# Kernel optimization log

Hardware: AMD Instinct MI355X
Metric: run time of the kernel (lower is better)

The kernel has to match this reference:

```python
import jax, jax.numpy as jnp
import numpy as np

M, H = 7, 200                 # ensemble size, hidden width
OBS, ACT = 32, 8
C = OBS + ACT                 # model input dim
DOUT = OBS + 1                # next-obs delta + reward
N = 100000                    # number of transitions
E_NUM = 5                     # number of elites
MAX_LOGVAR, MIN_LOGVAR = 0.5, -10.0
REWARD_SCALE, REWARD_BIAS = 1.0, 0.0
TERM_THRESH = 50.0


def setup_inputs() -> dict:
    key = jax.random.key(0)
    ks = jax.random.split(key, 10)
    def w(k, shape, fan_in):
        return jax.random.normal(k, shape, jnp.float32) / np.float32(np.sqrt(fan_in))
    return {
        "observations": jax.random.normal(ks[0], (N, OBS), jnp.float32),
        "actions": jax.random.normal(ks[1], (N, ACT), jnp.float32),
        "scaler_mu": jax.random.normal(ks[2], (C,), jnp.float32) * 0.1,
        "scaler_std": jax.random.uniform(ks[3], (C,), jnp.float32, 0.5, 1.5),
        "W1": w(ks[4], (M, C, H), C), "b1": jnp.zeros((M, 1, H), jnp.float32),
        "W2": w(ks[5], (M, H, H), H), "b2": jnp.zeros((M, 1, H), jnp.float32),
        "W3": w(ks[6], (M, H, H), H), "b3": jnp.zeros((M, 1, H), jnp.float32),
        "W4": w(ks[7], (M, H, 2 * DOUT), H), "b4": jnp.zeros((M, 1, 2 * DOUT), jnp.float32),
        "elites": jnp.arange(E_NUM, dtype=jnp.int32),
    }


def _ensemble_mlp(z, W1, b1, W2, b2, W3, b3, W4, b4):
    # z: [M, R, C] -> mean, logvar: [M, R, DOUT]
    h = jax.nn.swish(jnp.einsum('mrc,mch->mrh', z, W1) + b1)
    h = jax.nn.swish(jnp.einsum('mrh,mhk->mrk', h, W2) + b2)
    h = jax.nn.swish(jnp.einsum('mrh,mhk->mrk', h, W3) + b3)
    out = jnp.einsum('mrh,mhk->mrk', h, W4) + b4
    mean, logvar = out[..., :DOUT], out[..., DOUT:]
    logvar = MAX_LOGVAR - jax.nn.softplus(MAX_LOGVAR - logvar)
    logvar = MIN_LOGVAR + jax.nn.softplus(logvar - MIN_LOGVAR)
    return mean, logvar


def _terminal_fn(observations, actions, next_obs):
    # simple environment-style terminal predicate, shape [N, 1]
    return jnp.linalg.norm(next_obs, axis=-1, keepdims=True) > TERM_THRESH


def reference(observations, actions, scaler_mu, scaler_std,
              W1, b1, W2, b2, W3, b3, W4, b4, elites):
    key = jax.random.key(0)  # source uses the SAME key for permutation and noise
    z = jnp.concatenate([observations, actions], axis=1)
    z = (z - scaler_mu) / scaler_std
    n, c = z.shape
    e = elites.shape[0]
    r = (n - 1) // e + 1
    pad = e * r - n
    z = jnp.concatenate([z, jnp.zeros((pad, c), z.dtype)], axis=0)
    idxs = jax.random.permutation(key, e * r)
    tmp = z[idxs].reshape(e, r, c)                    # dispatch to elite slots
    zf = jnp.zeros((M, r, c), z.dtype).at[elites].set(tmp)
    mean, logvar = _ensemble_mlp(zf, W1, b1, W2, b2, W3, b3, W4, b4)
    std = jnp.exp(0.5 * logvar)
    ensemble_samples = mean + jax.random.normal(key, mean.shape) * std
    res = ensemble_samples[elites].reshape(e * r, DOUT)   # gather elites back
    es = jnp.zeros((e * r, DOUT), res.dtype).at[idxs].set(res)[:n]  # inverse perm
    samples = jnp.concatenate([es[:, :-1] + observations, es[:, -1:]], axis=1)
    next_obs = samples[..., :-1]
    reward = samples[..., -1] * REWARD_SCALE + REWARD_BIAS
    terminal = _terminal_fn(observations, actions, next_obs).squeeze(1)
    return next_obs, reward, terminal
```

## Files before the change

kernel.cpp:

```cpp
#include <hip/hip_runtime.h>
#include <stdint.h>

#define N_TOT   100000
#define NPAD    100352
#define NBLK    196
#define EPB     512
#define HISTN   (NBLK * 256)
#define R_PER   20000
#define NOISE_HALF 2310000u
#define PERM_HALF  50000u

#define JAX_PARTITIONABLE 1

#define ROWS 32
#define RG_N 2
#define BPM  625
#define MLP_GRID (5 * BPM)
#define KST  200

#define L1_U4 1664
#define L2_U4 5824
#define L4_U4 2240
#define PM_U4 (L1_U4 + 2 * L2_U4 + L4_U4)
#define L1OFF 0
#define L2OFF L1_U4
#define L3OFF (L1_U4 + L2_U4)
#define L4OFF (L1_U4 + 2 * L2_U4)
#define WPB   19

using f32x4  = __attribute__((ext_vector_type(4))) float;
using bf16x8 = __attribute__((ext_vector_type(8))) short;

__host__ __device__ __forceinline__ uint32_t rotl32(uint32_t x, unsigned d) {
  return (x << d) | (x >> (32u - d));
}

__host__ __device__ inline void tf2x32(uint32_t k0, uint32_t k1,
                                       uint32_t x0, uint32_t x1,
                                       uint32_t& o0, uint32_t& o1) {
  uint32_t k2 = k0 ^ k1 ^ 0x1BD11BDAu;
  x0 += k0; x1 += k1;
#define TFR(R) { x0 += x1; x1 = rotl32(x1, R); x1 ^= x0; }
  TFR(13u) TFR(15u) TFR(26u) TFR(6u)
  x0 += k1; x1 += k2 + 1u;
  TFR(17u) TFR(29u) TFR(16u) TFR(24u)
  x0 += k2; x1 += k0 + 2u;
  TFR(13u) TFR(15u) TFR(26u) TFR(6u)
  x0 += k0; x1 += k1 + 3u;
  TFR(17u) TFR(29u) TFR(16u) TFR(24u)
  x0 += k1; x1 += k2 + 4u;
  TFR(13u) TFR(15u) TFR(26u) TFR(6u)
  x0 += k2; x1 += k0 + 5u;
#undef TFR
  o0 = x0; o1 = x1;
}

__host__ __device__ inline uint32_t jax_bits32(uint32_t k0, uint32_t k1,
                                               uint32_t idx, uint32_t half) {
#if JAX_PARTITIONABLE
  (void)half;
  uint32_t o0, o1; tf2x32(k0, k1, 0u, idx, o0, o1);
  return o0 ^ o1;
#else
  uint32_t o0, o1;
  if (idx < half) { tf2x32(k0, k1, idx, idx + half, o0, o1); return o0; }
  else            { tf2x32(k0, k1, idx - half, idx, o0, o1); return o1; }
#endif
}

static void jax_split_host(uint32_t k0, uint32_t k1,
                           uint32_t* nk, uint32_t* sk) {
#if JAX_PARTITIONABLE
  tf2x32(k0, k1, 0u, 0u, nk[0], nk[1]);
  tf2x32(k0, k1, 0u, 1u, sk[0], sk[1]);
#else
  uint32_t a0, a1, b0, b1;
  tf2x32(k0, k1, 0u, 2u, a0, a1);
  tf2x32(k0, k1, 1u, 3u, b0, b1);
  nk[0] = a0; nk[1] = b0;
  sk[0] = a1; sk[1] = b1;
#endif
}

__device__ __forceinline__ void split2(float e0, float e1,
                                       uint32_t& hi, uint32_t& lo) {
  uint32_t u0 = __float_as_uint(e0), u1 = __float_as_uint(e1);
  float f0 = __uint_as_float(u0 & 0xFFFF0000u);
  float f1 = __uint_as_float(u1 & 0xFFFF0000u);
  uint32_t l0 = __float_as_uint(e0 - f0) >> 16;
  uint32_t l1 = __float_as_uint(e1 - f1) >> 16;
  hi = (u1 & 0xFFFF0000u) | (u0 >> 16);
  lo = (l1 << 16) | l0;
}

__device__ __forceinline__ void split1(float x, unsigned short& h,
                                       unsigned short& l) {
  uint32_t u = __float_as_uint(x);
  float fh = __uint_as_float(u & 0xFFFF0000u);
  h = (unsigned short)(u >> 16);
  l = (unsigned short)(__float_as_uint(x - fh) >> 16);
}

__device__ __forceinline__ float rec1(unsigned short h, unsigned short l) {
  return __uint_as_float((uint32_t)h << 16) + __uint_as_float((uint32_t)l << 16);
}

__device__ __forceinline__ bf16x8 punu4(uint4 x) {
  union { uint4 u; bf16x8 v; } t;
  t.u = x;
  return t.v;
}

__device__ __forceinline__ float fast_rcp(float x) {
  float r;
  asm("v_rcp_f32 %0, %1" : "=v"(r) : "v"(x));
  return r;
}

__device__ __forceinline__ void wpack_one(int flat,
                                          const float* __restrict__ W1,
                                          const float* __restrict__ W2,
                                          const float* __restrict__ W3,
                                          const float* __restrict__ W4,
                                          uint4* __restrict__ wpH,
                                          uint4* __restrict__ wpL) {
  int m = flat / PM_U4;
  int rem = flat - m * PM_U4;
  const float* W; int KIN, KOUT, nch, loc;
  if (rem < L2OFF)      { W = W1 + (size_t)m * 40 * 200;  KIN = 40;  KOUT = 200; nch = 2; loc = rem; }
  else if (rem < L3OFF) { W = W2 + (size_t)m * 200 * 200; KIN = 200; KOUT = 200; nch = 7; loc = rem - L2OFF; }
  else if (rem < L4OFF) { W = W3 + (size_t)m * 200 * 200; KIN = 200; KOUT = 200; nch = 7; loc = rem - L3OFF; }
  else                  { W = W4 + (size_t)m * 200 * 66;  KIN = 200; KOUT = 66;  nch = 7; loc = rem - L4OFF; }
  int lane = loc & 63;
  int tc = loc >> 6;
  int ch = tc % nch;
  int t  = tc / nch;
  int g = lane >> 4, cr = lane & 15;
  int k0 = ch * 32 + g * 8;
  int col = t * 16 + cr;
  const bool ok = (k0 < KIN) && (col < KOUT);
  float w[8];
#pragma unroll
  for (int j = 0; j < 8; ++j)
    w[j] = ok ? W[(size_t)(k0 + j) * KOUT + col] : 0.f;
  uint32_t hi[4], lo[4];
#pragma unroll
  for (int d = 0; d < 4; ++d)
    split2(w[2 * d], w[2 * d + 1], hi[d], lo[d]);
  wpH[flat] = make_uint4(hi[0], hi[1], hi[2], hi[3]);
  wpL[flat] = make_uint4(lo[0], lo[1], lo[2], lo[3]);
}

__global__ __launch_bounds__(256) void k_pre(uint32_t kk0, uint32_t kk1,
                                             uint32_t* __restrict__ keys,
                                             uint32_t* __restrict__ vals,
                                             uint32_t* __restrict__ hist,
                                             uint32_t* __restrict__ histZ) {
  __shared__ uint32_t h[256];
  int tid = threadIdx.x;
  int b = blockIdx.x;
  h[tid] = 0;
  __syncthreads();
  uint32_t base = b * (uint32_t)EPB + tid * 2u;
  uint32_t kq[2], vq[2];
#pragma unroll
  for (int j = 0; j < 2; ++j) {
    uint32_t i = base + j;
    if (i < (uint32_t)N_TOT) {
      kq[j] = jax_bits32(kk0, kk1, i, PERM_HALF);
      vq[j] = i;
    } else {
      kq[j] = 0xFFFFFFFFu;
      vq[j] = 0xFFFFFFFFu;
    }
    atomicAdd(&h[kq[j] & 255u], 1u);
  }
  *(uint2*)(keys + base) = make_uint2(kq[0], kq[1]);
  *(uint2*)(vals + base) = make_uint2(vq[0], vq[1]);
  __syncthreads();
  hist[b * 256 + tid] = h[tid];
  histZ[b * 256 + tid] = 0;
}

template<bool GENNEXT, bool LAST>
__global__ __launch_bounds__(512) void k_scat(const uint32_t* __restrict__ keyIn,
                                              const uint32_t* __restrict__ valIn,
                                              uint32_t* __restrict__ keyOut,
                                              uint32_t* __restrict__ valOut,
                                              const uint32_t* __restrict__ histRaw,
                                              uint32_t* __restrict__ histNext,
                                              uint32_t* __restrict__ histZero,
                                              int shift, uint32_t nk0, uint32_t nk1,
                                              int wpass,
                                              const float* __restrict__ W1,
                                              const float* __restrict__ W2,
                                              const float* __restrict__ W3,
                                              const float* __restrict__ W4,
                                              uint4* __restrict__ wpH,
                                              uint4* __restrict__ wpL) {
  __shared__ uint32_t ptot[2][256];
  __shared__ uint32_t pbef[2][256];
  __shared__ uint32_t tot[256];
  __shared__ uint32_t bas[256];
  __shared__ uint32_t offD[256];
  __shared__ uint32_t dig[EPB];
  __shared__ uint32_t histc[8 * 256];
  const int b = blockIdx.x, tid = threadIdx.x;

  if (b >= NBLK) {
    int flat = (wpass * WPB + (b - NBLK)) * EPB + tid;
    if (flat < 5 * PM_U4)
      wpack_one(flat, W1, W2, W3, W4, wpH, wpL);
    return;
  }

  const uint32_t key = keyIn[b * EPB + tid];
  const uint32_t val = valIn[b * EPB + tid];

  {
    const int d8 = tid & 255;
    const int half = tid >> 8;
    uint32_t t = 0, before = 0;
    const int b0 = half * (NBLK / 2);
    for (int b2 = b0; b2 < b0 + NBLK / 2; ++b2) {
      uint32_t v2 = histRaw[b2 * 256 + d8];
      t += v2;
      before += (b2 < b) ? v2 : 0u;
    }
    ptot[half][d8] = t;
    pbef[half][d8] = before;
    __syncthreads();
    if (tid < 256) {
      uint32_t tt = ptot[0][tid] + ptot[1][tid];
      tot[tid] = tt;
      bas[tid] = tt;
    }
    __syncthreads();
    for (int off = 1; off < 256; off <<= 1) {
      uint32_t v = 0;
      if (tid < 256 && tid >= off) v = bas[tid - off];
      __syncthreads();
      if (tid < 256) bas[tid] += v;
      __syncthreads();
    }
    if (tid < 256)
      offD[tid] = bas[tid] - tot[tid] + pbef[0][tid] + pbef[1][tid];
  }

  const uint32_t d = (key >> shift) & 255u;
  const int cp = tid >> 6;
  for (int x = tid; x < 8 * 256; x += EPB) histc[x] = 0;
  __syncthreads();
  dig[tid] = d;
  atomicAdd(&histc[cp * 256 + d], 1u);
  __syncthreads();
  if (tid < 256) {
    uint32_t run = 0;
#pragma unroll
    for (int c = 0; c < 8; ++c) {
      uint32_t t = histc[c * 256 + tid];
      histc[c * 256 + tid] = run;
      run += t;
    }
  }
  __syncthreads();
  int c = 0;
  for (int p = cp * 64; p < tid; ++p)
    c += (dig[p] == d);
  const uint32_t rank = histc[cp * 256 + d] + (uint32_t)c;
  const uint32_t off = offD[d] + rank;
  valOut[off] = val;
  if (!LAST) {
    uint32_t nkey;
    int nshift;
    if (GENNEXT) {
      nkey = (off < (uint32_t)N_TOT) ? jax_bits32(nk0, nk1, off, PERM_HALF)
                                     : 0xFFFFFFFFu;
      nshift = 0;
    } else {
      nkey = key;
      nshift = shift + 8;
    }
    keyOut[off] = nkey;
    atomicAdd(&histNext[(off / EPB) * 256 + ((nkey >> nshift) & 255u)], 1u);
    if (tid < 256) histZero[b * 256 + tid] = 0;
  }
}

__device__ inline float softplusf(float x) {
  float ax = fabsf(x);
  float r = log1pf(expf(-ax));
  return (x > 0.f) ? x + r : r;
}

__device__ inline float erfinvf_approx(float x) {
  float w = -logf((1.0f - x) * (1.0f + x));
  float p;
  if (w < 5.0f) {
    w = w - 2.5f;
    p = 2.81022636e-08f;
    p = fmaf(p, w, 3.43273939e-07f);
    p = fmaf(p, w, -3.5233877e-06f);
    p = fmaf(p, w, -4.39150654e-06f);
    p = fmaf(p, w, 0.00021858087f);
    p = fmaf(p, w, -0.00125372503f);
    p = fmaf(p, w, -0.00417768164f);
    p = fmaf(p, w, 0.246640727f);
    p = fmaf(p, w, 1.50140941f);
  } else {
    w = sqrtf(w) - 3.0f;
    p = -0.000200214257f;
    p = fmaf(p, w, 0.000100950558f);
    p = fmaf(p, w, 0.00134934322f);
    p = fmaf(p, w, -0.00367342844f);
    p = fmaf(p, w, 0.00573950773f);
    p = fmaf(p, w, -0.0076224613f);
    p = fmaf(p, w, 0.00943887047f);
    p = fmaf(p, w, 1.00167406f);
    p = fmaf(p, w, 2.83297682f);
  }
  return p * x;
}

template<int KOUT, int NTILES, int NCH, bool ACTV>
__device__ __forceinline__ void layer_mfma(unsigned short* __restrict__ Ahi,
                                           unsigned short* __restrict__ Alo,
                                           const uint4* __restrict__ wpH,
                                           const uint4* __restrict__ wpL,
                                           int woff,
                                           const float* __restrict__ bm,
                                           int wv, int lane) {
  constexpr int MAXT = (NTILES + 3) / 4;
  const int g  = lane >> 4;
  const int cr = lane & 15;
  f32x4 acc[RG_N][MAXT];
#pragma unroll
  for (int rg = 0; rg < RG_N; ++rg)
#pragma unroll
    for (int ti = 0; ti < MAXT; ++ti)
      acc[rg][ti] = (f32x4){0.f, 0.f, 0.f, 0.f};

  for (int ch = 0; ch < NCH; ++ch) {
    const int k0 = ch * 32 + g * 8;
    const bool ok = (k0 + 8 <= KST);
    const int ka = ok ? k0 : 0;
    uint4 hfa[RG_N], lfa[RG_N];
#pragma unroll
    for (int rg = 0; rg < RG_N; ++rg) {
      uint4 h = *(const uint4*)(Ahi + (rg * 16 + cr) * KST + ka);
      uint4 l = *(const uint4*)(Alo + (rg * 16 + cr) * KST + ka);
      if (!ok) { h = make_uint4(0, 0, 0, 0); l = make_uint4(0, 0, 0, 0); }
      hfa[rg] = h; lfa[rg] = l;
    }
#pragma unroll
    for (int ti = 0; ti < MAXT; ++ti) {
      const int t = wv + ti * 4;
      if (t < NTILES) {
        const int idx = woff + (t * NCH + ch) * 64 + lane;
        bf16x8 vbh = punu4(wpH[idx]);
        bf16x8 vbl = punu4(wpL[idx]);
#pragma unroll
        for (int rg = 0; rg < RG_N; ++rg) {
          bf16x8 vah = punu4(hfa[rg]);
          bf16x8 val = punu4(lfa[rg]);
          acc[rg][ti] = __builtin_amdgcn_mfma_f32_16x16x32_bf16(vah, vbh, acc[rg][ti], 0, 0, 0);
          acc[rg][ti] = __builtin_amdgcn_mfma_f32_16x16x32_bf16(val, vbh, acc[rg][ti], 0, 0, 0);
          acc[rg][ti] = __builtin_amdgcn_mfma_f32_16x16x32_bf16(vah, vbl, acc[rg][ti], 0, 0, 0);
        }
      }
    }
  }
  __syncthreads();
#pragma unroll
  for (int ti = 0; ti < MAXT; ++ti) {
    const int t = wv + ti * 4;
    if (t < NTILES) {
      const int col = t * 16 + cr;
      if (col < KOUT) {
        const float bias = bm[col];
#pragma unroll
        for (int rg = 0; rg < RG_N; ++rg) {
#pragma unroll
          for (int rr = 0; rr < 4; ++rr) {
            float x = acc[rg][ti][rr] + bias;
            if (ACTV) x = x * fast_rcp(1.0f + expf(-x));
            unsigned short h, l;
            split1(x, h, l);
            const int row = rg * 16 + g * 4 + rr;
            Ahi[row * KST + col] = h;
            Alo[row * KST + col] = l;
          }
        }
      }
    }
  }
  __syncthreads();
}

__global__ __launch_bounds__(256, 6) void k_mlp(
    const float* __restrict__ obs, const float* __restrict__ act,
    const float* __restrict__ mu, const float* __restrict__ sst,
    const uint4* __restrict__ wpH, const uint4* __restrict__ wpL,
    const float* __restrict__ b1, const float* __restrict__ b2,
    const float* __restrict__ b3, const float* __restrict__ b4,
    const uint32_t* __restrict__ idxs, float* __restrict__ outv) {
  __shared__ __align__(16) unsigned short Ahi[ROWS * KST];
  __shared__ __align__(16) unsigned short Alo[ROWS * KST];
  __shared__ uint32_t jrow[ROWS];
  __shared__ float nrm[ROWS];
  __shared__ float muv[40];
  __shared__ float rsd[40];
  const int tid = threadIdx.x;
  const int m  = blockIdx.x / BPM;
  const int bb = blockIdx.x - m * BPM;
  const int i0 = m * R_PER + bb * ROWS;
  const int wv = tid >> 6;
  const int lane = tid & 63;
  const int mw = m * PM_U4;

  if (tid < ROWS) {
    jrow[tid] = idxs[i0 + tid];
    nrm[tid] = 0.f;
  }
  if (tid >= 64 && tid < 104) {
    int cc = tid - 64;
    muv[cc] = mu[cc];
    rsd[cc] = 1.0f / sst[cc];
  }
  __syncthreads();

  for (int t = tid; t < ROWS * 64; t += 256) {
    int rr = t >> 6, cc = t & 63;
    float v = 0.f;
    if (cc < 40) {
      uint32_t j = jrow[rr];
      float x = (cc < 32) ? obs[(size_t)j * 32 + cc] : act[(size_t)j * 8 + (cc - 32)];
      v = (x - muv[cc]) * rsd[cc];
    }
    unsigned short h, l;
    split1(v, h, l);
    Ahi[rr * KST + cc] = h;
    Alo[rr * KST + cc] = l;
  }
  __syncthreads();

  layer_mfma<200, 13, 2, true >(Ahi, Alo, wpH, wpL, mw + L1OFF, b1 + (size_t)m * 200, wv, lane);
  layer_mfma<200, 13, 7, true >(Ahi, Alo, wpH, wpL, mw + L2OFF, b2 + (size_t)m * 200, wv, lane);
  layer_mfma<200, 13, 7, true >(Ahi, Alo, wpH, wpL, mw + L3OFF, b3 + (size_t)m * 200, wv, lane);
  layer_mfma< 66,  5, 7, false>(Ahi, Alo, wpH, wpL, mw + L4OFF, b4 + (size_t)m * 66, wv, lane);

  float* onext = outv;
  float* orew  = outv + 3200000;
  float* oterm = outv + 3300000;

  for (int t = tid; t < ROWS * 33; t += 256) {
    int rw = t / 33, kc = t - rw * 33;
    float mean = rec1(Ahi[rw * KST + kc],      Alo[rw * KST + kc]);
    float lvr  = rec1(Ahi[rw * KST + 33 + kc], Alo[rw * KST + 33 + kc]);
    float lv = 0.5f - softplusf(0.5f - lvr);
    lv = -10.0f + softplusf(lv + 10.0f);
    float sd = expf(0.5f * lv);
    int q = bb * ROWS + rw;
    uint32_t tno = (uint32_t)(m * 660000 + q * 33 + kc);
    uint32_t bits = jax_bits32(0u, 0u, tno, NOISE_HALF);
    float f = __uint_as_float((bits >> 9) | 0x3F800000u) - 1.0f;
    const float LOu = -0.99999994f;
    float u = fmaxf(LOu, fmaf(f, 2.0f, LOu));
    float nz = 1.41421356237f * erfinvf_approx(u);
    float s = mean + nz * sd;
    uint32_t j = jrow[rw];
    if (kc < 32) {
      float no = s + obs[(size_t)j * 32 + kc];
      onext[(size_t)j * 32 + kc] = no;
      atomicAdd(&nrm[rw], no * no);
    } else {
      orew[j] = s;
    }
  }
  __syncthreads();
  if (tid < ROWS) {
    uint32_t j = jrow[tid];
    oterm[j] = (sqrtf(nrm[tid]) > 50.0f) ? 1.0f : 0.0f;
  }
}

extern "C" void kernel_launch(void* const* d_in, const int* in_sizes, int n_in,
                              void* d_out, int out_size, void* d_ws, size_t ws_size,
                              hipStream_t stream) {
  (void)in_sizes; (void)n_in; (void)out_size; (void)ws_size;
  const float* obs = (const float*)d_in[0];
  const float* act = (const float*)d_in[1];
  const float* mu  = (const float*)d_in[2];
  const float* sst = (const float*)d_in[3];
  const float* W1  = (const float*)d_in[4];
  const float* b1  = (const float*)d_in[5];
  const float* W2  = (const float*)d_in[6];
  const float* b2  = (const float*)d_in[7];
  const float* W3  = (const float*)d_in[8];
  const float* b3  = (const float*)d_in[9];
  const float* W4  = (const float*)d_in[10];
  const float* b4  = (const float*)d_in[11];

  uint8_t* ws = (uint8_t*)d_ws;
  uint32_t* keysA = (uint32_t*)(ws);
  uint32_t* keysB = (uint32_t*)(ws + 401408);
  uint32_t* valsA = (uint32_t*)(ws + 802816);
  uint32_t* valsB = (uint32_t*)(ws + 1204224);
  uint32_t* hA    = (uint32_t*)(ws + 1605632);
  uint32_t* hB    = (uint32_t*)(ws + 1806336);
  uint32_t* hC    = (uint32_t*)(ws + 2007040);
  uint4*    wpH   = (uint4*)(ws + 2207744);
  uint4*    wpL   = (uint4*)(ws + 3451904);

  uint32_t key0[2] = {0u, 0u}, key1[2], sub1[2], key2[2], sub2[2];
  jax_split_host(key0[0], key0[1], key1, sub1);
  jax_split_host(key1[0], key1[1], key2, sub2);

  dim3 gs(NBLK + WPB), blk(256), blk512(512);

  k_pre<<<dim3(NBLK), blk, 0, stream>>>(sub1[0], sub1[1], keysA, valsA, hA, hB);
  k_scat<false,false><<<gs, blk512, 0, stream>>>(keysA, valsA, keysB, valsB, hA, hB, hC, 0,  0u, 0u, 0, W1, W2, W3, W4, wpH, wpL);
  k_scat<false,false><<<gs, blk512, 0, stream>>>(keysB, valsB, keysA, valsA, hB, hC, hA, 8,  0u, 0u, 1, W1, W2, W3, W4, wpH, wpL);
  k_scat<false,false><<<gs, blk512, 0, stream>>>(keysA, valsA, keysB, valsB, hC, hA, hB, 16, 0u, 0u, 2, W1, W2, W3, W4, wpH, wpL);
  k_scat<true, false><<<gs, blk512, 0, stream>>>(keysB, valsB, keysA, valsA, hA, hB, hC, 24, sub2[0], sub2[1], 3, W1, W2, W3, W4, wpH, wpL);
  k_scat<false,false><<<gs, blk512, 0, stream>>>(keysA, valsA, keysB, valsB, hB, hC, hA, 0,  0u, 0u, 4, W1, W2, W3, W4, wpH, wpL);
  k_scat<false,false><<<gs, blk512, 0, stream>>>(keysB, valsB, keysA, valsA, hC, hA, hB, 8,  0u, 0u, 5, W1, W2, W3, W4, wpH, wpL);
  k_scat<false,false><<<gs, blk512, 0, stream>>>(keysA, valsA, keysB, valsB, hA, hB, hC, 16, 0u, 0u, 6, W1, W2, W3, W4, wpH, wpL);
  k_scat<false,true ><<<gs, blk512, 0, stream>>>(keysB, valsB, keysA, valsA, hB, hC, hA, 24, 0u, 0u, 7, W1, W2, W3, W4, wpH, wpL);

  k_mlp<<<dim3(MLP_GRID), blk, 0, stream>>>(obs, act, mu, sst,
                                            wpH, wpL, b1, b2, b3, b4,
                                            valsA, (float*)d_out);
}
```

Baseline: 303.0 us.

## Precompute Gaussian noise in spare radix-sort blocks and read it in MLP epilogue

Adds extra blocks to each radix-sort scatter launch that precompute the threefry-based Gaussian noise into a workspace buffer, one slice per pass. The MLP epilogue then loads the noise from memory instead of computing the hash and erfinv inline. The aim is to move the RNG work off the critical MLP kernel and overlap it with the latency-bound sort passes. In exchange it writes and reads about 13 MB of extra memory, and it falls back to inline computation when the workspace is too small.

```diff
diff --git a/kernel.cpp b/kernel.cpp
--- a/kernel.cpp
+++ b/kernel.cpp
@@ -9,6 +9,8 @@
 #define R_PER   20000
 #define NOISE_HALF 2310000u
 #define PERM_HALF  50000u
+#define NZ_TOT  3300000u
+#define NZ_SLICE 412500u
 
 #define JAX_PARTITIONABLE 1
 
@@ -27,6 +29,7 @@
 #define L3OFF (L1_U4 + L2_U4)
 #define L4OFF (L1_U4 + 2 * L2_U4)
 #define WPB   19
+#define NZB   41
 
 using f32x4  = __attribute__((ext_vector_type(4))) float;
 using bf16x8 = __attribute__((ext_vector_type(8))) short;
@@ -115,182 +118,6 @@
   float r;
   asm("v_rcp_f32 %0, %1" : "=v"(r) : "v"(x));
   return r;
-}
-
-__device__ __forceinline__ void wpack_one(int flat,
-                                          const float* __restrict__ W1,
-                                          const float* __restrict__ W2,
-                                          const float* __restrict__ W3,
-                                          const float* __restrict__ W4,
-                                          uint4* __restrict__ wpH,
-                                          uint4* __restrict__ wpL) {
-  int m = flat / PM_U4;
-  int rem = flat - m * PM_U4;
-  const float* W; int KIN, KOUT, nch, loc;
-  if (rem < L2OFF)      { W = W1 + (size_t)m * 40 * 200;  KIN = 40;  KOUT = 200; nch = 2; loc = rem; }
-  else if (rem < L3OFF) { W = W2 + (size_t)m * 200 * 200; KIN = 200; KOUT = 200; nch = 7; loc = rem - L2OFF; }
-  else if (rem < L4OFF) { W = W3 + (size_t)m * 200 * 200; KIN = 200; KOUT = 200; nch = 7; loc = rem - L3OFF; }
-  else                  { W = W4 + (size_t)m * 200 * 66;  KIN = 200; KOUT = 66;  nch = 7; loc = rem - L4OFF; }
-  int lane = loc & 63;
-  int tc = loc >> 6;
-  int ch = tc % nch;
-  int t  = tc / nch;
-  int g = lane >> 4, cr = lane & 15;
-  int k0 = ch * 32 + g * 8;
-  int col = t * 16 + cr;
-  const bool ok = (k0 < KIN) && (col < KOUT);
-  float w[8];
-#pragma unroll
-  for (int j = 0; j < 8; ++j)
-    w[j] = ok ? W[(size_t)(k0 + j) * KOUT + col] : 0.f;
-  uint32_t hi[4], lo[4];
-#pragma unroll
-  for (int d = 0; d < 4; ++d)
-    split2(w[2 * d], w[2 * d + 1], hi[d], lo[d]);
-  wpH[flat] = make_uint4(hi[0], hi[1], hi[2], hi[3]);
-  wpL[flat] = make_uint4(lo[0], lo[1], lo[2], lo[3]);
-}
-
-__global__ __launch_bounds__(256) void k_pre(uint32_t kk0, uint32_t kk1,
-                                             uint32_t* __restrict__ keys,
-                                             uint32_t* __restrict__ vals,
-                                             uint32_t* __restrict__ hist,
-                                             uint32_t* __restrict__ histZ) {
-  __shared__ uint32_t h[256];
-  int tid = threadIdx.x;
-  int b = blockIdx.x;
-  h[tid] = 0;
-  __syncthreads();
-  uint32_t base = b * (uint32_t)EPB + tid * 2u;
-  uint32_t kq[2], vq[2];
-#pragma unroll
-  for (int j = 0; j < 2; ++j) {
-    uint32_t i = base + j;
-    if (i < (uint32_t)N_TOT) {
-      kq[j] = jax_bits32(kk0, kk1, i, PERM_HALF);
-      vq[j] = i;
-    } else {
-      kq[j] = 0xFFFFFFFFu;
-      vq[j] = 0xFFFFFFFFu;
-    }
-    atomicAdd(&h[kq[j] & 255u], 1u);
-  }
-  *(uint2*)(keys + base) = make_uint2(kq[0], kq[1]);
-  *(uint2*)(vals + base) = make_uint2(vq[0], vq[1]);
-  __syncthreads();
-  hist[b * 256 + tid] = h[tid];
-  histZ[b * 256 + tid] = 0;
-}
-
-template<bool GENNEXT, bool LAST>
-__global__ __launch_bounds__(512) void k_scat(const uint32_t* __restrict__ keyIn,
-                                              const uint32_t* __restrict__ valIn,
-                                              uint32_t* __restrict__ keyOut,
-                                              uint32_t* __restrict__ valOut,
-                                              const uint32_t* __restrict__ histRaw,
-                                              uint32_t* __restrict__ histNext,
-                                              uint32_t* __restrict__ histZero,
-                                              int shift, uint32_t nk0, uint32_t nk1,
-                                              int wpass,
-                                              const float* __restrict__ W1,
-                                              const float* __restrict__ W2,
-                                              const float* __restrict__ W3,
-                                              const float* __restrict__ W4,
-                                              uint4* __restrict__ wpH,
-                                              uint4* __restrict__ wpL) {
-  __shared__ uint32_t ptot[2][256];
-  __shared__ uint32_t pbef[2][256];
-  __shared__ uint32_t tot[256];
-  __shared__ uint32_t bas[256];
-  __shared__ uint32_t offD[256];
-  __shared__ uint32_t dig[EPB];
-  __shared__ uint32_t histc[8 * 256];
-  const int b = blockIdx.x, tid = threadIdx.x;
-
-  if (b >= NBLK) {
-    int flat = (wpass * WPB + (b - NBLK)) * EPB + tid;
-    if (flat < 5 * PM_U4)
-      wpack_one(flat, W1, W2, W3, W4, wpH, wpL);
-    return;
-  }
-
-  const uint32_t key = keyIn[b * EPB + tid];
-  const uint32_t val = valIn[b * EPB + tid];
-
-  {
-    const int d8 = tid & 255;
-    const int half = tid >> 8;
-    uint32_t t = 0, before = 0;
-    const int b0 = half * (NBLK / 2);
-    for (int b2 = b0; b2 < b0 + NBLK / 2; ++b2) {
-      uint32_t v2 = histRaw[b2 * 256 + d8];
-      t += v2;
-      before += (b2 < b) ? v2 : 0u;
-    }
-    ptot[half][d8] = t;
-    pbef[half][d8] = before;
-    __syncthreads();
-    if (tid < 256) {
-      uint32_t tt = ptot[0][tid] + ptot[1][tid];
-      tot[tid] = tt;
-      bas[tid] = tt;
-    }
-    __syncthreads();
-    for (int off = 1; off < 256; off <<= 1) {
-      uint32_t v = 0;
-      if (tid < 256 && tid >= off) v = bas[tid - off];
-      __syncthreads();
-      if (tid < 256) bas[tid] += v;
-      __syncthreads();
-    }
-    if (tid < 256)
-      offD[tid] = bas[tid] - tot[tid] + pbef[0][tid] + pbef[1][tid];
-  }
-
-  const uint32_t d = (key >> shift) & 255u;
-  const int cp = tid >> 6;
-  for (int x = tid; x < 8 * 256; x += EPB) histc[x] = 0;
-  __syncthreads();
-  dig[tid] = d;
-  atomicAdd(&histc[cp * 256 + d], 1u);
-  __syncthreads();
-  if (tid < 256) {
-    uint32_t run = 0;
-#pragma unroll
-    for (int c = 0; c < 8; ++c) {
-      uint32_t t = histc[c * 256 + tid];
-      histc[c * 256 + tid] = run;
-      run += t;
-    }
-  }
-  __syncthreads();
-  int c = 0;
-  for (int p = cp * 64; p < tid; ++p)
-    c += (dig[p] == d);
-  const uint32_t rank = histc[cp * 256 + d] + (uint32_t)c;
-  const uint32_t off = offD[d] + rank;
-  valOut[off] = val;
-  if (!LAST) {
-    uint32_t nkey;
-    int nshift;
-    if (GENNEXT) {
-      nkey = (off < (uint32_t)N_TOT) ? jax_bits32(nk0, nk1, off, PERM_HALF)
-                                     : 0xFFFFFFFFu;
-      nshift = 0;
-    } else {
-      nkey = key;
-      nshift = shift + 8;
-    }
-    keyOut[off] = nkey;
-    atomicAdd(&histNext[(off / EPB) * 256 + ((nkey >> nshift) & 255u)], 1u);
-    if (tid < 256) histZero[b * 256 + tid] = 0;
-  }
-}
-
-__device__ inline float softplusf(float x) {
-  float ax = fabsf(x);
-  float r = log1pf(expf(-ax));
-  return (x > 0.f) ? x + r : r;
 }
 
 __device__ inline float erfinvf_approx(float x) {
@@ -322,6 +149,199 @@
   return p * x;
 }
 
+__device__ __forceinline__ float noise_at(uint32_t tno) {
+  uint32_t bits = jax_bits32(0u, 0u, tno, NOISE_HALF);
+  float f = __uint_as_float((bits >> 9) | 0x3F800000u) - 1.0f;
+  const float LOu = -0.99999994f;
+  float u = fmaxf(LOu, fmaf(f, 2.0f, LOu));
+  return 1.41421356237f * erfinvf_approx(u);
+}
+
+__device__ __forceinline__ void wpack_one(int flat,
+                                          const float* __restrict__ W1,
+                                          const float* __restrict__ W2,
+                                          const float* __restrict__ W3,
+                                          const float* __restrict__ W4,
+                                          uint4* __restrict__ wpH,
+                                          uint4* __restrict__ wpL) {
+  int m = flat / PM_U4;
+  int rem = flat - m * PM_U4;
+  const float* W; int KIN, KOUT, nch, loc;
+  if (rem < L2OFF)      { W = W1 + (size_t)m * 40 * 200;  KIN = 40;  KOUT = 200; nch = 2; loc = rem; }
+  else if (rem < L3OFF) { W = W2 + (size_t)m * 200 * 200; KIN = 200; KOUT = 200; nch = 7; loc = rem - L2OFF; }
+  else if (rem < L4OFF) { W = W3 + (size_t)m * 200 * 200; KIN = 200; KOUT = 200; nch = 7; loc = rem - L3OFF; }
+  else                  { W = W4 + (size_t)m * 200 * 66;  KIN = 200; KOUT = 66;  nch = 7; loc = rem - L4OFF; }
+  int lane = loc & 63;
+  int tc = loc >> 6;
+  int ch = tc % nch;
+  int t  = tc / nch;
+  int g = lane >> 4, cr = lane & 15;
+  int k0 = ch * 32 + g * 8;
+  int col = t * 16 + cr;
+  const bool ok = (k0 < KIN) && (col < KOUT);
+  float w[8];
+#pragma unroll
+  for (int j = 0; j < 8; ++j)
+    w[j] = ok ? W[(size_t)(k0 + j) * KOUT + col] : 0.f;
+  uint32_t hi[4], lo[4];
+#pragma unroll
+  for (int d = 0; d < 4; ++d)
+    split2(w[2 * d], w[2 * d + 1], hi[d], lo[d]);
+  wpH[flat] = make_uint4(hi[0], hi[1], hi[2], hi[3]);
+  wpL[flat] = make_uint4(lo[0], lo[1], lo[2], lo[3]);
+}
+
+__global__ __launch_bounds__(256) void k_pre(uint32_t kk0, uint32_t kk1,
+                                             uint32_t* __restrict__ keys,
+                                             uint32_t* __restrict__ vals,
+                                             uint32_t* __restrict__ hist,
+                                             uint32_t* __restrict__ histZ) {
+  __shared__ uint32_t h[256];
+  int tid = threadIdx.x;
+  int b = blockIdx.x;
+  h[tid] = 0;
+  __syncthreads();
+  uint32_t base = b * (uint32_t)EPB + tid * 2u;
+  uint32_t kq[2], vq[2];
+#pragma unroll
+  for (int j = 0; j < 2; ++j) {
+    uint32_t i = base + j;
+    if (i < (uint32_t)N_TOT) {
+      kq[j] = jax_bits32(kk0, kk1, i, PERM_HALF);
+      vq[j] = i;
+    } else {
+      kq[j] = 0xFFFFFFFFu;
+      vq[j] = 0xFFFFFFFFu;
+    }
+    atomicAdd(&h[kq[j] & 255u], 1u);
+  }
+  *(uint2*)(keys + base) = make_uint2(kq[0], kq[1]);
+  *(uint2*)(vals + base) = make_uint2(vq[0], vq[1]);
+  __syncthreads();
+  hist[b * 256 + tid] = h[tid];
+  histZ[b * 256 + tid] = 0;
+}
+
+template<bool GENNEXT, bool LAST>
+__global__ __launch_bounds__(512) void k_scat(const uint32_t* __restrict__ keyIn,
+                                              const uint32_t* __restrict__ valIn,
+                                              uint32_t* __restrict__ keyOut,
+                                              uint32_t* __restrict__ valOut,
+                                              const uint32_t* __restrict__ histRaw,
+                                              uint32_t* __restrict__ histNext,
+                                              uint32_t* __restrict__ histZero,
+                                              int shift, uint32_t nk0, uint32_t nk1,
+                                              int wpass,
+                                              const float* __restrict__ W1,
+                                              const float* __restrict__ W2,
+                                              const float* __restrict__ W3,
+                                              const float* __restrict__ W4,
+                                              uint4* __restrict__ wpH,
+                                              uint4* __restrict__ wpL,
+                                              float* __restrict__ nzbuf) {
+  __shared__ uint32_t ptot[2][256];
+  __shared__ uint32_t pbef[2][256];
+  __shared__ uint32_t tot[256];
+  __shared__ uint32_t bas[256];
+  __shared__ uint32_t offD[256];
+  __shared__ uint32_t dig[EPB];
+  __shared__ uint32_t histc[8 * 256];
+  const int b = blockIdx.x, tid = threadIdx.x;
+
+  if (b >= NBLK + WPB) {
+    const uint32_t lo = (uint32_t)wpass * NZ_SLICE;
+    const uint32_t hi = lo + NZ_SLICE;
+    for (uint32_t i = lo + (uint32_t)(b - NBLK - WPB) * EPB + tid;
+         i < hi; i += (uint32_t)NZB * EPB)
+      nzbuf[i] = noise_at(i);
+    return;
+  }
+  if (b >= NBLK) {
+    int flat = (wpass * WPB + (b - NBLK)) * EPB + tid;
+    if (flat < 5 * PM_U4)
+      wpack_one(flat, W1, W2, W3, W4, wpH, wpL);
+    return;
+  }
+
+  const uint32_t key = keyIn[b * EPB + tid];
+  const uint32_t val = valIn[b * EPB + tid];
+
+  {
+    const int d8 = tid & 255;
+    const int half = tid >> 8;
+    uint32_t t = 0, before = 0;
+    const int b0 = half * (NBLK / 2);
+    for (int b2 = b0; b2 < b0 + NBLK / 2; ++b2) {
+      uint32_t v2 = histRaw[b2 * 256 + d8];
+      t += v2;
+      before += (b2 < b) ? v2 : 0u;
+    }
+    ptot[half][d8] = t;
+    pbef[half][d8] = before;
+    __syncthreads();
+    if (tid < 256) {
+      uint32_t tt = ptot[0][tid] + ptot[1][tid];
+      tot[tid] = tt;
+      bas[tid] = tt;
+    }
+    __syncthreads();
+    for (int off = 1; off < 256; off <<= 1) {
+      uint32_t v = 0;
+      if (tid < 256 && tid >= off) v = bas[tid - off];
+      __syncthreads();
+      if (tid < 256) bas[tid] += v;
+      __syncthreads();
+    }
+    if (tid < 256)
+      offD[tid] = bas[tid] - tot[tid] + pbef[0][tid] + pbef[1][tid];
+  }
+
+  const uint32_t d = (key >> shift) & 255u;
+  const int cp = tid >> 6;
+  for (int x = tid; x < 8 * 256; x += EPB) histc[x] = 0;
+  __syncthreads();
+  dig[tid] = d;
+  atomicAdd(&histc[cp * 256 + d], 1u);
+  __syncthreads();
+  if (tid < 256) {
+    uint32_t run = 0;
+#pragma unroll
+    for (int c = 0; c < 8; ++c) {
+      uint32_t t = histc[c * 256 + tid];
+      histc[c * 256 + tid] = run;
+      run += t;
+    }
+  }
+  __syncthreads();
+  int c = 0;
+  for (int p = cp * 64; p < tid; ++p)
+    c += (dig[p] == d);
+  const uint32_t rank = histc[cp * 256 + d] + (uint32_t)c;
+  const uint32_t off = offD[d] + rank;
+  valOut[off] = val;
+  if (!LAST) {
+    uint32_t nkey;
+    int nshift;
+    if (GENNEXT) {
+      nkey = (off < (uint32_t)N_TOT) ? jax_bits32(nk0, nk1, off, PERM_HALF)
+                                     : 0xFFFFFFFFu;
+      nshift = 0;
+    } else {
+      nkey = key;
+      nshift = shift + 8;
+    }
+    keyOut[off] = nkey;
+    atomicAdd(&histNext[(off / EPB) * 256 + ((nkey >> nshift) & 255u)], 1u);
+    if (tid < 256) histZero[b * 256 + tid] = 0;
+  }
+}
+
+__device__ inline float softplusf(float x) {
+  float ax = fabsf(x);
+  float r = log1pf(expf(-ax));
+  return (x > 0.f) ? x + r : r;
+}
+
 template<int KOUT, int NTILES, int NCH, bool ACTV>
 __device__ __forceinline__ void layer_mfma(unsigned short* __restrict__ Ahi,
                                            unsigned short* __restrict__ Alo,
@@ -403,7 +423,8 @@
     const uint4* __restrict__ wpH, const uint4* __restrict__ wpL,
     const float* __restrict__ b1, const float* __restrict__ b2,
     const float* __restrict__ b3, const float* __restrict__ b4,
-    const uint32_t* __restrict__ idxs, float* __restrict__ outv) {
+    const uint32_t* __restrict__ idxs, const float* __restrict__ nzbuf,
+    float* __restrict__ outv) {
   __shared__ __align__(16) unsigned short Ahi[ROWS * KST];
   __shared__ __align__(16) unsigned short Alo[ROWS * KST];
   __shared__ uint32_t jrow[ROWS];
@@ -462,11 +483,7 @@
     float sd = expf(0.5f * lv);
     int q = bb * ROWS + rw;
     uint32_t tno = (uint32_t)(m * 660000 + q * 33 + kc);
-    uint32_t bits = jax_bits32(0u, 0u, tno, NOISE_HALF);
-    float f = __uint_as_float((bits >> 9) | 0x3F800000u) - 1.0f;
-    const float LOu = -0.99999994f;
-    float u = fmaxf(LOu, fmaf(f, 2.0f, LOu));
-    float nz = 1.41421356237f * erfinvf_approx(u);
+    float nz = nzbuf ? nzbuf[tno] : noise_at(tno);
     float s = mean + nz * sd;
     uint32_t j = jrow[rw];
     if (kc < 32) {
@@ -487,7 +504,7 @@
 extern "C" void kernel_launch(void* const* d_in, const int* in_sizes, int n_in,
                               void* d_out, int out_size, void* d_ws, size_t ws_size,
                               hipStream_t stream) {
-  (void)in_sizes; (void)n_in; (void)out_size; (void)ws_size;
+  (void)in_sizes; (void)n_in; (void)out_size;
   const float* obs = (const float*)d_in[0];
   const float* act = (const float*)d_in[1];
   const float* mu  = (const float*)d_in[2];
@@ -511,24 +528,28 @@
   uint32_t* hC    = (uint32_t*)(ws + 2007040);
   uint4*    wpH   = (uint4*)(ws + 2207744);
   uint4*    wpL   = (uint4*)(ws + 3451904);
+  const size_t NZ_OFF = 4696064;
+  const size_t WS_NEED = NZ_OFF + (size_t)NZ_TOT * 4;
+  float* nzbuf = (ws_size >= WS_NEED) ? (float*)(ws + NZ_OFF) : nullptr;
 
   uint32_t key0[2] = {0u, 0u}, key1[2], sub1[2], key2[2], sub2[2];
   jax_split_host(key0[0], key0[1], key1, sub1);
   jax_split_host(key1[0], key1[1], key2, sub2);
 
-  dim3 gs(NBLK + WPB), blk(256), blk512(512);
+  const int extra = nzbuf ? (WPB + NZB) : WPB;
+  dim3 gs(NBLK + extra), blk(256), blk512(512);
 
   k_pre<<<dim3(NBLK), blk, 0, stream>>>(sub1[0], sub1[1], keysA, valsA, hA, hB);
-  k_scat<false,false><<<gs, blk512, 0, stream>>>(keysA, valsA, keysB, valsB, hA, hB, hC, 0,  0u, 0u, 0, W1, W2, W3, W4, wpH, wpL);
-  k_scat<false,false><<<gs, blk512, 0, stream>>>(keysB, valsB, keysA, valsA, hB, hC, hA, 8,  0u, 0u, 1, W1, W2, W3, W4, wpH, wpL);
-  k_scat<false,false><<<gs, blk512, 0, stream>>>(keysA, valsA, keysB, valsB, hC, hA, hB, 16, 0u, 0u, 2, W1, W2, W3, W4, wpH, wpL);
-  k_scat<true, false><<<gs, blk512, 0, stream>>>(keysB, valsB, keysA, valsA, hA, hB, hC, 24, sub2[0], sub2[1], 3, W1, W2, W3, W4, wpH, wpL);
-  k_scat<false,false><<<gs, blk512, 0, stream>>>(keysA, valsA, keysB, valsB, hB, hC, hA, 0,  0u, 0u, 4, W1, W2, W3, W4, wpH, wpL);
-  k_scat<false,false><<<gs, blk512, 0, stream>>>(keysB, valsB, keysA, valsA, hC, hA, hB, 8,  0u, 0u, 5, W1, W2, W3, W4, wpH, wpL);
-  k_scat<false,false><<<gs, blk512, 0, stream>>>(keysA, valsA, keysB, valsB, hA, hB, hC, 16, 0u, 0u, 6, W1, W2, W3, W4, wpH, wpL);
-  k_scat<false,true ><<<gs, blk512, 0, stream>>>(keysB, valsB, keysA, valsA, hB, hC, hA, 24, 0u, 0u, 7, W1, W2, W3, W4, wpH, wpL);
+  k_scat<false,false><<<gs, blk512, 0, stream>>>(keysA, valsA, keysB, valsB, hA, hB, hC, 0,  0u, 0u, 0, W1, W2, W3, W4, wpH, wpL, nzbuf);
+  k_scat<false,false><<<gs, blk512, 0, stream>>>(keysB, valsB, keysA, valsA, hB, hC, hA, 8,  0u, 0u, 1, W1, W2, W3, W4, wpH, wpL, nzbuf);
+  k_scat<false,false><<<gs, blk512, 0, stream>>>(keysA, valsA, keysB, valsB, hC, hA, hB, 16, 0u, 0u, 2, W1, W2, W3, W4, wpH, wpL, nzbuf);
+  k_scat<true, false><<<gs, blk512, 0, stream>>>(keysB, valsB, keysA, valsA, hA, hB, hC, 24, sub2[0], sub2[1], 3, W1, W2, W3, W4, wpH, wpL, nzbuf);
+  k_scat<false,false><<<gs, blk512, 0, stream>>>(keysA, valsA, keysB, valsB, hB, hC, hA, 0,  0u, 0u, 4, W1, W2, W3, W4, wpH, wpL, nzbuf);
+  k_scat<false,false><<<gs, blk512, 0, stream>>>(keysB, valsB, keysA, valsA, hC, hA, hB, 8,  0u, 0u, 5, W1, W2, W3, W4, wpH, wpL, nzbuf);
+  k_scat<false,false><<<gs, blk512, 0, stream>>>(keysA, valsA, keysB, valsB, hA, hB, hC, 16, 0u, 0u, 6, W1, W2, W3, W4, wpH, wpL, nzbuf);
+  k_scat<false,true ><<<gs, blk512, 0, stream>>>(keysB, valsB, keysA, valsA, hB, hC, hA, 24, 0u, 0u, 7, W1, W2, W3, W4, wpH, wpL, nzbuf);
 
   k_mlp<<<dim3(MLP_GRID), blk, 0, stream>>>(obs, act, mu, sst,
                                             wpH, wpL, b1, b2, b3, b4,
-                                            valsA, (float*)d_out);
-}
+                                            valsA, nzbuf, (float*)d_out);
+}
```

Measured after the change: 315.3 us. 4.0% more time.
